# Kernel tuning notes

Measured on AMD Instinct MI355X. Metric: run time of the kernel, lower is better.

The kernel has to match this reference:

```python
import jax, jax.numpy as jnp
import numpy as np

N_HEADS = 12

def setup_inputs() -> dict:
    key = jax.random.key(0)
    k1, k2, k3 = jax.random.split(key, 3)
    B, N, D = 2, 2048, 768
    x = jax.random.normal(k1, (B, N, D), dtype=jnp.float32)
    # Linear weights stored as [in, out] (equivalent to torch W.T)
    Wkqv = jax.random.normal(k2, (D, 3 * D), dtype=jnp.float32) * (1.0 / np.sqrt(D))
    bkqv = jnp.zeros((3 * D,), dtype=jnp.float32)
    Wproj = jax.random.normal(k3, (D, D), dtype=jnp.float32) * (1.0 / np.sqrt(D))
    bproj = jnp.zeros((D,), dtype=jnp.float32)
    return {"x": x, "Wkqv": Wkqv, "bkqv": bkqv, "Wproj": Wproj, "bproj": bproj}


def reference(x, Wkqv, bkqv, Wproj, bproj):
    B, N, D = x.shape
    H = N_HEADS
    hd = D // H
    kqv = x @ Wkqv + bkqv                     # [B, N, 3D]
    # NOTE: original chunks in (k, q, v) order
    k, q, v = jnp.split(kqv, 3, axis=-1)
    k = k.reshape(B, N, H, hd).transpose(0, 2, 1, 3)   # [B, H, N, hd]
    q = q.reshape(B, N, H, hd).transpose(0, 2, 1, 3)
    v = v.reshape(B, N, H, hd).transpose(0, 2, 1, 3)
    att = jnp.einsum('bhqd,bhkd->bhqk', q, k) / jnp.sqrt(jnp.float32(hd))
    causal = jnp.tril(jnp.ones((N, N), dtype=bool))    # [N, N]
    att = jnp.where(causal[None, None, :, :], att, jnp.float32(-jnp.inf))
    w = jax.nn.softmax(att, axis=-1)
    sa = jnp.einsum('bhqk,bhkd->bhqd', w, v)           # [B, H, N, hd]
    sa = sa.transpose(0, 2, 1, 3).reshape(B, N, D)
    return sa @ Wproj + bproj
```

## Files before the change

### kernel.cpp

```cpp
#include <hip/hip_runtime.h>

typedef __attribute__((ext_vector_type(8))) short bf16x8;
typedef __attribute__((ext_vector_type(4))) float f32x4;
typedef __attribute__((ext_vector_type(16))) float f32x16;

#define BATCH 2
#define SEQ 2048
#define DMODEL 768
#define NH 12
#define HD 64
#define M_TOK (BATCH * SEQ)
#define N_KQV (3 * DMODEL)

#define GLOAD16(gsrc, ldst) __builtin_amdgcn_global_load_lds( \
    (const __attribute__((address_space(1))) unsigned int*)(const void*)(gsrc), \
    (__attribute__((address_space(3))) unsigned int*)(void*)(ldst), 16, 0, 0)

__device__ __forceinline__ unsigned short f2bf(float f) {
  unsigned int u = __float_as_uint(f);
  u += 0x7FFFu + ((u >> 16) & 1u);
  return (unsigned short)(u >> 16);
}

__device__ __forceinline__ unsigned int cvtpk(float lo, float hi) {
  unsigned int r;
  asm("v_cvt_pk_bf16_f32 %0, %1, %2" : "=v"(r) : "v"(lo), "v"(hi));
  return r;
}


__global__ void cvt_f32_bf16(const float* __restrict__ in,
                             unsigned short* __restrict__ out, int n4) {
  int i = blockIdx.x * blockDim.x + threadIdx.x;
  if (i >= n4) return;
  float4 v = reinterpret_cast<const float4*>(in)[i];
  unsigned long long p = (unsigned long long)f2bf(v.x)
                       | ((unsigned long long)f2bf(v.y) << 16)
                       | ((unsigned long long)f2bf(v.z) << 32)
                       | ((unsigned long long)f2bf(v.w) << 48);
  reinterpret_cast<unsigned long long*>(out)[i] = p;
}

__global__ void transpose_cvt(const float* __restrict__ in,
                              unsigned short* __restrict__ out,
                              int rows, int cols) {
  __shared__ float tile[32][33];
  int c0 = blockIdx.x * 32, r0 = blockIdx.y * 32;
  for (int i = threadIdx.y; i < 32; i += 8)
    tile[i][threadIdx.x] = in[(size_t)(r0 + i) * cols + c0 + threadIdx.x];
  __syncthreads();
  for (int i = threadIdx.y; i < 32; i += 8)
    out[(size_t)(c0 + i) * rows + r0 + threadIdx.x] = f2bf(tile[threadIdx.x][i]);
}

template <int BM, int BN, int MODE>
__global__ __launch_bounds__(256) void gemm_bt(
    const unsigned short* __restrict__ A,
    const unsigned short* __restrict__ BT,
    const float* __restrict__ bias,
    int M, int N, int K,
    unsigned short* __restrict__ outK, unsigned short* __restrict__ outQ,
    unsigned short* __restrict__ outVT, float* __restrict__ outF) {
  constexpr int MI = BM / 64;
  constexpr int NJ = BN / 64;
  constexpr int L = BM / 64 + BN / 64;
  __shared__ __align__(16) unsigned short lds_a[2][BM][32];
  __shared__ __align__(16) unsigned short lds_b[2][BN][32];
  const int tid = threadIdx.x;
  const int lane = tid & 63;
  const int w = tid >> 6;
  const int wm = w >> 1, wn = w & 1;
  const int l31 = lane & 31, hi = lane >> 5;
  const int m0 = blockIdx.y * BM, n0 = blockIdx.x * BN;

  f32x16 acc[MI][NJ];
#pragma unroll
  for (int mi = 0; mi < MI; mi++)
#pragma unroll
    for (int nj = 0; nj < NJ; nj++)
#pragma unroll
      for (int i = 0; i < 16; i++) acc[mi][nj][i] = 0.f;

  const int srow = lane >> 2;
  const int sg = ((lane & 3) ^ ((lane >> 3) & 3)) * 8;
  const int xq = (l31 >> 1) & 3;

#define STAGE(buf, k0)                                                        \
  {                                                                           \
    _Pragma("unroll")                                                         \
    for (int rr = 0; rr < BM / 64; ++rr)                                      \
      GLOAD16(&A[(size_t)(m0 + rr * 64 + w * 16 + srow) * K + (k0) + sg],     \
              &lds_a[buf][rr * 64 + w * 16][0]);                              \
    _Pragma("unroll")                                                         \
    for (int rr = 0; rr < BN / 64; ++rr)                                      \
      GLOAD16(&BT[(size_t)(n0 + rr * 64 + w * 16 + srow) * K + (k0) + sg],    \
              &lds_b[buf][rr * 64 + w * 16][0]);                              \
  }

  const int KT = K >> 5;
  STAGE(0, 0);
  STAGE(1, 32);

  for (int kt = 0; kt < KT; ++kt) {
    const int cur = kt & 1;
    if (kt + 1 < KT) {
      if constexpr (L == 4)      asm volatile("s_waitcnt vmcnt(4)" ::: "memory");
      else if constexpr (L == 3) asm volatile("s_waitcnt vmcnt(3)" ::: "memory");
      else                       asm volatile("s_waitcnt vmcnt(2)" ::: "memory");
    } else {
      asm volatile("s_waitcnt vmcnt(0)" ::: "memory");
    }
    __builtin_amdgcn_s_barrier();
    __builtin_amdgcn_sched_barrier(0);

    bf16x8 aA[2][MI], aB[2][NJ];
#pragma unroll
    for (int ds = 0; ds < 2; ds++) {
      const int rc = ((ds * 2 + hi) ^ xq) * 8;
#pragma unroll
      for (int mi = 0; mi < MI; mi++)
        aA[ds][mi] = *(const bf16x8*)&lds_a[cur][wm * (BM / 2) + mi * 32 + l31][rc];
#pragma unroll
      for (int nj = 0; nj < NJ; nj++)
        aB[ds][nj] = *(const bf16x8*)&lds_b[cur][wn * (BN / 2) + nj * 32 + l31][rc];
    }
#pragma unroll
    for (int ds = 0; ds < 2; ds++)
#pragma unroll
      for (int mi = 0; mi < MI; mi++)
#pragma unroll
        for (int nj = 0; nj < NJ; nj++)
          acc[mi][nj] = __builtin_amdgcn_mfma_f32_32x32x16_bf16(
              aA[ds][mi], aB[ds][nj], acc[mi][nj], 0, 0, 0);

    __builtin_amdgcn_s_barrier();
    if (kt + 2 < KT) STAGE(cur, (kt + 2) << 5);
  }
#undef STAGE

#pragma unroll
  for (int mi = 0; mi < MI; mi++) {
#pragma unroll
    for (int nj = 0; nj < NJ; nj++) {
#pragma unroll
      for (int r = 0; r < 16; r++) {
        int row = m0 + wm * (BM / 2) + mi * 32 + (r & 3) + 8 * (r >> 2) + 4 * hi;
        int col = n0 + wn * (BN / 2) + nj * 32 + l31;
        float v = acc[mi][nj][r] + bias[col];
        if (MODE == 0) {
          int chunk = col / DMODEL;
          int d = col - chunk * DMODEL;
          int hh = d >> 6, di = d & 63;
          int bb = row >> 11, tok = row & 2047;
          int bh = bb * NH + hh;
          if (chunk == 0)
            outK[((size_t)bh * SEQ + tok) * HD + di] = f2bf(v);
          else if (chunk == 1)
            outQ[((size_t)bh * SEQ + tok) * HD + di] = f2bf(v * 0.125f);
          else
            outVT[((size_t)bh * HD + di) * SEQ + tok] = f2bf(v);
        } else {
          outF[(size_t)row * N + col] = v;
        }
      }
    }
  }
}

__global__ __launch_bounds__(128) void attn_kernel(
    const unsigned short* __restrict__ qbuf,
    const unsigned short* __restrict__ kbuf,
    const unsigned short* __restrict__ vT,
    unsigned short* __restrict__ sa) {
  __shared__ __align__(16) char smem_raw[18432];
  auto k_lds = reinterpret_cast<unsigned short (*)[72]>(smem_raw);
  auto v_lds = reinterpret_cast<unsigned short (*)[72]>(smem_raw + 9216);
  auto o_merge = reinterpret_cast<float (*)[32][33]>(smem_raw);
  auto l_merge = reinterpret_cast<float (*)[32]>(smem_raw + 9216);

  const int tid = threadIdx.x, lane = tid & 63, w = tid >> 6;
  const int l31 = lane & 31, hi = lane >> 5;

  const int fid = (int)blockIdx.y * (int)gridDim.x + (int)blockIdx.x;
  const int xcd = fid & 7, slot = fid >> 3;
  const int head3 = slot % 3;
  const int t = 63 - slot / 3;
  const int bh = head3 * 8 + xcd;
  const int ktmax = t >> 1;

  const size_t qk_base = (size_t)bh * SEQ * HD;
  const size_t v_base = (size_t)bh * HD * SEQ;
  const int bb = bh / NH, h = bh - bb * NH;

  const int sr = w * 32 + (lane >> 3);
  const int sc = (lane & 7) * 8;

  {
    bf16x8 rk[4], rv[4];
#pragma unroll
    for (int p = 0; p < 4; p++) {
      rk[p] = *(const bf16x8*)&kbuf[qk_base + (size_t)(sr + 8 * p) * HD + sc];
      rv[p] = *(const bf16x8*)&vT[v_base + (size_t)(sr + 8 * p) * SEQ + sc];
    }
#pragma unroll
    for (int p = 0; p < 4; p++) {
      *(bf16x8*)&k_lds[sr + 8 * p][sc] = rk[p];
      *(bf16x8*)&v_lds[sr + 8 * p][sc] = rv[p];
    }
  }

  bf16x8 aq[4];
#pragma unroll
  for (int ds = 0; ds < 4; ds++)
    aq[ds] = *(const bf16x8*)&qbuf[qk_base + (size_t)(t * 32 + l31) * HD + ds * 16 + hi * 8];

  f32x16 o0, o1;
#pragma unroll
  for (int i = 0; i < 16; i++) { o0[i] = 0.f; o1[i] = 0.f; }
  float lsum = 0.f;

  __syncthreads();

  for (int kt = 0; kt <= ktmax; ++kt) {
    const bool more = (kt < ktmax);
    bf16x8 rk[4], rv[4];
    if (more) {
      const int nrow = (kt + 1) * 64;
#pragma unroll
      for (int p = 0; p < 4; p++) {
        rk[p] = *(const bf16x8*)&kbuf[qk_base + (size_t)(nrow + sr + 8 * p) * HD + sc];
        rv[p] = *(const bf16x8*)&vT[v_base + (size_t)(sr + 8 * p) * SEQ + nrow + sc];
      }
    }

    f32x16 s;
#pragma unroll
    for (int i = 0; i < 16; i++) s[i] = 0.f;
    __builtin_amdgcn_s_setprio(1);
#pragma unroll
    for (int ds = 0; ds < 4; ds++) {
      bf16x8 bk = *(const bf16x8*)&k_lds[w * 32 + l31][ds * 16 + hi * 8];
      s = __builtin_amdgcn_mfma_f32_32x32x16_bf16(bk, aq[ds], s, 0, 0, 0);
    }
    __builtin_amdgcn_s_setprio(0);

    const bool diag = (kt == ktmax);
    const int qb2 = (t & 1) * 32;
#pragma unroll
    for (int r = 0; r < 16; r++) {
      int kr = (r & 3) + 8 * (r >> 2) + 4 * hi;
      float val = s[r];
      if (diag && (w * 32 + kr > qb2 + l31)) val = -1e30f;
      float p = __expf(val);
      s[r] = p;
      lsum += p;
    }

    union { unsigned int u[4]; bf16x8 v; } f1, f2;
    {
      unsigned int A = cvtpk(s[0], s[1]), B = cvtpk(s[2], s[3]);
      unsigned int C = cvtpk(s[4], s[5]), D = cvtpk(s[6], s[7]);
      auto rAC = __builtin_amdgcn_permlane32_swap(A, C, false, false);
      auto rBD = __builtin_amdgcn_permlane32_swap(B, D, false, false);
      f1.u[0] = rAC[0]; f1.u[1] = rBD[0]; f1.u[2] = rAC[1]; f1.u[3] = rBD[1];
      unsigned int A2 = cvtpk(s[8], s[9]),   B2 = cvtpk(s[10], s[11]);
      unsigned int C2 = cvtpk(s[12], s[13]), D2 = cvtpk(s[14], s[15]);
      auto rAC2 = __builtin_amdgcn_permlane32_swap(A2, C2, false, false);
      auto rBD2 = __builtin_amdgcn_permlane32_swap(B2, D2, false, false);
      f2.u[0] = rAC2[0]; f2.u[1] = rBD2[0]; f2.u[2] = rAC2[1]; f2.u[3] = rBD2[1];
    }

    __builtin_amdgcn_s_setprio(1);
    {
      bf16x8 bv00 = *(const bf16x8*)&v_lds[l31][w * 32 + hi * 8];
      bf16x8 bv01 = *(const bf16x8*)&v_lds[32 + l31][w * 32 + hi * 8];
      o0 = __builtin_amdgcn_mfma_f32_32x32x16_bf16(f1.v, bv00, o0, 0, 0, 0);
      o1 = __builtin_amdgcn_mfma_f32_32x32x16_bf16(f1.v, bv01, o1, 0, 0, 0);
      bf16x8 bv10 = *(const bf16x8*)&v_lds[l31][w * 32 + 16 + hi * 8];
      bf16x8 bv11 = *(const bf16x8*)&v_lds[32 + l31][w * 32 + 16 + hi * 8];
      o0 = __builtin_amdgcn_mfma_f32_32x32x16_bf16(f2.v, bv10, o0, 0, 0, 0);
      o1 = __builtin_amdgcn_mfma_f32_32x32x16_bf16(f2.v, bv11, o1, 0, 0, 0);
    }
    __builtin_amdgcn_s_setprio(0);

    if (more) {
      __syncthreads();
#pragma unroll
      for (int p = 0; p < 4; p++) {
        *(bf16x8*)&k_lds[sr + 8 * p][sc] = rk[p];
        *(bf16x8*)&v_lds[sr + 8 * p][sc] = rv[p];
      }
      __syncthreads();
    }
  }

  __syncthreads();
  {
    float ltot = lsum + __shfl_xor(lsum, 32);
    if (hi == 0) l_merge[w][l31] = ltot;
    f32x16 osend = w ? o0 : o1;
#pragma unroll
    for (int r = 0; r < 16; r++) {
      int ql = (r & 3) + 8 * (r >> 2) + 4 * hi;
      o_merge[w][ql][l31] = osend[r];
    }
    __syncthreads();
    f32x16 okeep = w ? o1 : o0;
#pragma unroll
    for (int r = 0; r < 16; r++) {
      int ql = (r & 3) + 8 * (r >> 2) + 4 * hi;
      float ot = okeep[r] + o_merge[1 - w][ql][l31];
      float lt = l_merge[0][ql] + l_merge[1][ql];
      sa[((size_t)bb * SEQ + t * 32 + ql) * DMODEL + h * HD + w * 32 + l31] = f2bf(ot / lt);
    }
  }
}


extern "C" void kernel_launch(void* const* d_in, const int* in_sizes, int n_in,
                              void* d_out, int out_size, void* d_ws, size_t ws_size,
                              hipStream_t stream) {
  const float* x     = (const float*)d_in[0];
  const float* Wkqv  = (const float*)d_in[1];
  const float* bkqv  = (const float*)d_in[2];
  const float* Wproj = (const float*)d_in[3];
  const float* bproj = (const float*)d_in[4];
  float* out = (float*)d_out;

  char* ws = (char*)d_ws;
  unsigned short* x_bf   = (unsigned short*)(ws + 0);
  unsigned short* wkqvT  = (unsigned short*)(ws + 6291456);
  unsigned short* wprojT = (unsigned short*)(ws + 9830400);
  unsigned short* qb     = (unsigned short*)(ws + 11010048);
  unsigned short* kb     = (unsigned short*)(ws + 17301504);
  unsigned short* vT     = (unsigned short*)(ws + 23592960);
  unsigned short* sa     = (unsigned short*)(ws + 29884416);

  cvt_f32_bf16<<<(M_TOK * DMODEL / 4 + 255) / 256, 256, 0, stream>>>(x, x_bf, M_TOK * DMODEL / 4);
  transpose_cvt<<<dim3(N_KQV / 32, DMODEL / 32), dim3(32, 8), 0, stream>>>(Wkqv, wkqvT, DMODEL, N_KQV);
  transpose_cvt<<<dim3(DMODEL / 32, DMODEL / 32), dim3(32, 8), 0, stream>>>(Wproj, wprojT, DMODEL, DMODEL);

  gemm_bt<128, 128, 0><<<dim3(N_KQV / 128, M_TOK / 128), 256, 0, stream>>>(
      x_bf, wkqvT, bkqv, M_TOK, N_KQV, DMODEL, kb, qb, vT, nullptr);

  attn_kernel<<<dim3(64, BATCH * NH), 128, 0, stream>>>(qb, kb, vT, sa);

  gemm_bt<64, 64, 1><<<dim3(DMODEL / 64, M_TOK / 64), 256, 0, stream>>>(
      sa, wprojT, bproj, M_TOK, DMODEL, DMODEL, nullptr, nullptr, nullptr, out);
}
```

Measured before the change: 107.9 us.

## Merge prep kernels into one launch and triple-buffer GEMM LDS to drop barrier

Result: faster. 103.0 us (-4.5%).

```diff
diff --git a/kernel.cpp b/kernel.cpp
--- a/kernel.cpp
+++ b/kernel.cpp
@@ -28,29 +28,45 @@
   return r;
 }
 
-
-__global__ void cvt_f32_bf16(const float* __restrict__ in,
-                             unsigned short* __restrict__ out, int n4) {
-  int i = blockIdx.x * blockDim.x + threadIdx.x;
-  if (i >= n4) return;
-  float4 v = reinterpret_cast<const float4*>(in)[i];
-  unsigned long long p = (unsigned long long)f2bf(v.x)
-                       | ((unsigned long long)f2bf(v.y) << 16)
-                       | ((unsigned long long)f2bf(v.z) << 32)
-                       | ((unsigned long long)f2bf(v.w) << 48);
-  reinterpret_cast<unsigned long long*>(out)[i] = p;
-}
-
-__global__ void transpose_cvt(const float* __restrict__ in,
-                              unsigned short* __restrict__ out,
-                              int rows, int cols) {
+#define NB_CVT 3072
+#define NB_T1 (72 * 24)
+#define NB_T2 (24 * 24)
+
+__global__ __launch_bounds__(256) void prep_kernel(
+    const float* __restrict__ x, unsigned short* __restrict__ x_bf,
+    const float* __restrict__ Wkqv, unsigned short* __restrict__ wkqvT,
+    const float* __restrict__ Wproj, unsigned short* __restrict__ wprojT) {
+  const int b = blockIdx.x;
+  if (b < NB_CVT) {
+    int i = b * 256 + threadIdx.x;
+    float4 v = reinterpret_cast<const float4*>(x)[i];
+    unsigned long long p = (unsigned long long)f2bf(v.x)
+                         | ((unsigned long long)f2bf(v.y) << 16)
+                         | ((unsigned long long)f2bf(v.z) << 32)
+                         | ((unsigned long long)f2bf(v.w) << 48);
+    reinterpret_cast<unsigned long long*>(x_bf)[i] = p;
+    return;
+  }
   __shared__ float tile[32][33];
-  int c0 = blockIdx.x * 32, r0 = blockIdx.y * 32;
-  for (int i = threadIdx.y; i < 32; i += 8)
-    tile[i][threadIdx.x] = in[(size_t)(r0 + i) * cols + c0 + threadIdx.x];
+  const float* in;
+  unsigned short* out;
+  int rows, cols, bx, by;
+  if (b < NB_CVT + NB_T1) {
+    int j = b - NB_CVT;
+    in = Wkqv; out = wkqvT; rows = DMODEL; cols = N_KQV;
+    bx = j % 72; by = j / 72;
+  } else {
+    int j = b - NB_CVT - NB_T1;
+    in = Wproj; out = wprojT; rows = DMODEL; cols = DMODEL;
+    bx = j % 24; by = j / 24;
+  }
+  const int tx = threadIdx.x & 31, ty = threadIdx.x >> 5;
+  int c0 = bx * 32, r0 = by * 32;
+  for (int i = ty; i < 32; i += 8)
+    tile[i][tx] = in[(size_t)(r0 + i) * cols + c0 + tx];
   __syncthreads();
-  for (int i = threadIdx.y; i < 32; i += 8)
-    out[(size_t)(c0 + i) * rows + r0 + threadIdx.x] = f2bf(tile[threadIdx.x][i]);
+  for (int i = ty; i < 32; i += 8)
+    out[(size_t)(c0 + i) * rows + r0 + tx] = f2bf(tile[tx][i]);
 }
 
 template <int BM, int BN, int MODE>
@@ -64,8 +80,8 @@
   constexpr int MI = BM / 64;
   constexpr int NJ = BN / 64;
   constexpr int L = BM / 64 + BN / 64;
-  __shared__ __align__(16) unsigned short lds_a[2][BM][32];
-  __shared__ __align__(16) unsigned short lds_b[2][BN][32];
+  __shared__ __align__(16) unsigned short lds_a[3][BM][32];
+  __shared__ __align__(16) unsigned short lds_b[3][BN][32];
   const int tid = threadIdx.x;
   const int lane = tid & 63;
   const int w = tid >> 6;
@@ -101,8 +117,8 @@
   STAGE(0, 0);
   STAGE(1, 32);
 
+  int cur = 0;
   for (int kt = 0; kt < KT; ++kt) {
-    const int cur = kt & 1;
     if (kt + 1 < KT) {
       if constexpr (L == 4)      asm volatile("s_waitcnt vmcnt(4)" ::: "memory");
       else if constexpr (L == 3) asm volatile("s_waitcnt vmcnt(3)" ::: "memory");
@@ -133,8 +149,11 @@
           acc[mi][nj] = __builtin_amdgcn_mfma_f32_32x32x16_bf16(
               aA[ds][mi], aB[ds][nj], acc[mi][nj], 0, 0, 0);
 
-    __builtin_amdgcn_s_barrier();
-    if (kt + 2 < KT) STAGE(cur, (kt + 2) << 5);
+    if (kt + 2 < KT) {
+      const int nb = (cur + 2 >= 3) ? cur - 1 : cur + 2;
+      STAGE(nb, (kt + 2) << 5);
+    }
+    cur = (cur == 2) ? 0 : cur + 1;
   }
 #undef STAGE
 
@@ -336,9 +355,8 @@
   unsigned short* vT     = (unsigned short*)(ws + 23592960);
   unsigned short* sa     = (unsigned short*)(ws + 29884416);
 
-  cvt_f32_bf16<<<(M_TOK * DMODEL / 4 + 255) / 256, 256, 0, stream>>>(x, x_bf, M_TOK * DMODEL / 4);
-  transpose_cvt<<<dim3(N_KQV / 32, DMODEL / 32), dim3(32, 8), 0, stream>>>(Wkqv, wkqvT, DMODEL, N_KQV);
-  transpose_cvt<<<dim3(DMODEL / 32, DMODEL / 32), dim3(32, 8), 0, stream>>>(Wproj, wprojT, DMODEL, DMODEL);
+  prep_kernel<<<NB_CVT + NB_T1 + NB_T2, 256, 0, stream>>>(
+      x, x_bf, Wkqv, wkqvT, Wproj, wprojT);
 
   gemm_bt<128, 128, 0><<<dim3(N_KQV / 128, M_TOK / 128), 256, 0, stream>>>(
       x_bf, wkqvT, bkqv, M_TOK, N_KQV, DMODEL, kb, qb, vT, nullptr);
```
